# Performance work log

Measured on AMD Instinct MI355X. Metric: run time of the kernel, lower is better.

Reference implementation:

```python
import jax, jax.numpy as jnp
import numpy as np

N = 100000      # nodes
E = 1600000     # edges
IN = 128        # in_channels
HID = 32        # hidden_channels
HEADS = 4
G = 256         # number of graphs in the batch
NEG_SLOPE = 0.2


def setup_inputs() -> dict:
    key = jax.random.key(0)
    ks = jax.random.split(key, 20)
    s = 0.1
    d = {
        'x': jax.random.normal(ks[0], (N, IN), jnp.float32),
        'edge_index': jax.random.randint(ks[1], (2, E), 0, N, dtype=jnp.int64),
        'batch': jnp.sort(jax.random.randint(ks[2], (N,), 0, G, dtype=jnp.int64)),
        # conv1: IN -> HID per head, HEADS heads, concat
        'W1': jax.random.normal(ks[3], (IN, HEADS * HID), jnp.float32) * s,
        'a_src1': jax.random.normal(ks[4], (HEADS, HID), jnp.float32) * s,
        'a_dst1': jax.random.normal(ks[5], (HEADS, HID), jnp.float32) * s,
        'b1': jnp.zeros((HEADS * HID,), jnp.float32),
        # conv2: HEADS*HID -> HID per head, HEADS heads, concat
        'W2': jax.random.normal(ks[6], (HEADS * HID, HEADS * HID), jnp.float32) * s,
        'a_src2': jax.random.normal(ks[7], (HEADS, HID), jnp.float32) * s,
        'a_dst2': jax.random.normal(ks[8], (HEADS, HID), jnp.float32) * s,
        'b2': jnp.zeros((HEADS * HID,), jnp.float32),
        # conv3: HEADS*HID -> HID, 1 head, no concat (mean over heads is identity)
        'W3': jax.random.normal(ks[9], (HEADS * HID, HID), jnp.float32) * s,
        'a_src3': jax.random.normal(ks[10], (1, HID), jnp.float32) * s,
        'a_dst3': jax.random.normal(ks[11], (1, HID), jnp.float32) * s,
        'b3': jnp.zeros((HID,), jnp.float32),
        # final readout
        'fc_w': jax.random.normal(ks[12], (HID, 1), jnp.float32) * s,
        'fc_b': jnp.zeros((1,), jnp.float32),
    }
    return d


def _gat_layer(x, src, dst, W, a_s, a_d, b, concat):
    """One PyG-style GATConv: edge attention logits, per-destination softmax, scatter-aggregate."""
    n = x.shape[0]
    H, C = a_s.shape
    h = (x @ W).reshape(n, H, C)                       # [N, H, C]
    asrc = (h * a_s).sum(-1)                           # [N, H]
    adst = (h * a_d).sum(-1)                           # [N, H]
    e = jax.nn.leaky_relu(asrc[src] + adst[dst], NEG_SLOPE)   # [Etot, H]
    m = jax.ops.segment_max(e, dst, num_segments=n)    # per-dst max (self-loops guarantee non-empty)
    ex = jnp.exp(e - m[dst])
    den = jax.ops.segment_sum(ex, dst, num_segments=n)
    alpha = ex / (den[dst] + 1e-16)                    # segment softmax, [Etot, H]
    out = jax.ops.segment_sum(alpha[:, :, None] * h[src], dst, num_segments=n)  # [N, H, C]
    if concat:
        return out.reshape(n, H * C) + b
    return out.mean(axis=1) + b


def reference(x, edge_index, batch, W1, a_src1, a_dst1, b1, W2, a_src2, a_dst2, b2,
              W3, a_src3, a_dst3, b3, fc_w, fc_b):
    n = x.shape[0]
    loops = jnp.arange(n, dtype=edge_index.dtype)      # GATConv adds self-loops by default
    src = jnp.concatenate([edge_index[0], loops])
    dst = jnp.concatenate([edge_index[1], loops])

    h = jax.nn.elu(_gat_layer(x, src, dst, W1, a_src1, a_dst1, b1, True))
    h = jax.nn.elu(_gat_layer(h, src, dst, W2, a_src2, a_dst2, b2, True))
    h = jax.nn.elu(_gat_layer(h, src, dst, W3, a_src3, a_dst3, b3, False))

    counts = jax.ops.segment_sum(jnp.ones((n,), h.dtype), batch, num_segments=G)
    pooled = jax.ops.segment_sum(h, batch, num_segments=G) / jnp.maximum(counts, 1.0)[:, None]
    # dropout p=0.5 is identity in eval mode
    return pooled @ fc_w + fc_b                        # [G, 1]
```

## Files before the change

kernel.cpp:

```cpp
#include <hip/hip_runtime.h>
#include <hip/hip_bf16.h>
#include <math.h>

#define NEG_SLOPE 0.2f
#define CHUNK 6144

typedef short bf16x8 __attribute__((ext_vector_type(8)));
typedef float f32x4  __attribute__((ext_vector_type(4)));

__device__ __forceinline__ float leaky(float x){ return x > 0.f ? x : NEG_SLOPE*x; }
__device__ __forceinline__ float elu(float x){ return x > 0.f ? x : expm1f(x); }

__device__ __forceinline__ ushort f2bf(float f){
  uint u = __float_as_uint(f);
  u += 0x7fffu + ((u >> 16) & 1u);
  return (ushort)(u >> 16);
}
__device__ __forceinline__ uint pk2(float lo, float hi){
  return (uint)f2bf(lo) | ((uint)f2bf(hi) << 16);
}
__device__ __forceinline__ float2 bfpair(uint v){
  return make_float2(__uint_as_float(v << 16), __uint_as_float(v & 0xffff0000u));
}

__global__ __launch_bounds__(256) void k_histA(const int* __restrict__ ei, int E,
                                               int* __restrict__ bucketCount){
  __shared__ int hist[512];
  for (int b = threadIdx.x; b < 512; b += 256) hist[b] = 0;
  __syncthreads();
  int base = blockIdx.x * 2048;
  int cnt = min(2048, E - base);
  for (int i = threadIdx.x; i < cnt; i += 256)
    atomicAdd(&hist[ei[E + base + i] >> 8], 1);
  __syncthreads();
  for (int b = threadIdx.x; b < 512; b += 256)
    if (hist[b]) atomicAdd(&bucketCount[b], hist[b]);
}

__global__ __launch_bounds__(256) void k_scanB(const int* __restrict__ bucketCount, int NB,
                        int* __restrict__ bucketBase, int* __restrict__ gcursor, int E){
  __shared__ int s[512];
  for (int b = threadIdx.x; b < 512; b += 256)
    s[b] = (b < NB) ? bucketCount[b] : 0;
  __syncthreads();
  if (threadIdx.x == 0){
    int run = 0;
    for (int b = 0; b < NB; b++){ int v = s[b]; s[b] = run; run += v; }
  }
  __syncthreads();
  for (int b = threadIdx.x; b < NB; b += 256){
    bucketBase[b] = s[b]; gcursor[b] = s[b];
  }
  if (threadIdx.x == 0) bucketBase[NB] = E;
}

__global__ __launch_bounds__(256) void k_scatA(const int* __restrict__ ei, int E, int NB,
                         int* __restrict__ gcursor, uint* __restrict__ tmp){
  __shared__ uint stageS[CHUNK];
  __shared__ uint stageD[CHUNK];
  __shared__ int hist[512], pre[512], cur[512], gbase[512];
  __shared__ int scanArr[256];
  int tid = threadIdx.x;
  int base = blockIdx.x * CHUNK;
  int cnt = min(CHUNK, E - base);
  for (int b = tid; b < 512; b += 256) hist[b] = 0;
  __syncthreads();
  for (int i = tid; i < cnt; i += 256)
    atomicAdd(&hist[ei[E + base + i] >> 8], 1);
  __syncthreads();
  int a0 = hist[2*tid], a1 = hist[2*tid+1];
  scanArr[tid] = a0 + a1;
  __syncthreads();
  for (int st = 1; st < 256; st <<= 1){
    int v = (tid >= st) ? scanArr[tid - st] : 0;
    __syncthreads();
    scanArr[tid] += v;
    __syncthreads();
  }
  int eb = tid ? scanArr[tid-1] : 0;
  pre[2*tid] = eb;        cur[2*tid] = eb;
  pre[2*tid+1] = eb + a0; cur[2*tid+1] = eb + a0;
  if (2*tid < NB && a0 > 0)   gbase[2*tid]   = atomicAdd(&gcursor[2*tid],   a0);
  if (2*tid+1 < NB && a1 > 0) gbase[2*tid+1] = atomicAdd(&gcursor[2*tid+1], a1);
  __syncthreads();
  for (int i = tid; i < cnt; i += 256){
    int s = ei[base + i];
    int d = ei[E + base + i];
    int lpos = atomicAdd(&cur[d >> 8], 1);
    stageS[lpos] = (uint)s; stageD[lpos] = (uint)d;
  }
  __syncthreads();
  for (int i = tid; i < cnt; i += 256){
    uint d = stageD[i];
    int b = d >> 8;
    tmp[gbase[b] + (i - pre[b])] = (stageS[i] << 8) | (d & 255u);
  }
}

__global__ __launch_bounds__(256) void k_csr(const uint* __restrict__ tmp,
                      const int* __restrict__ bucketBase,
                      int N, int NB, int* __restrict__ offsets, int* __restrict__ csr){
  int b = blockIdx.x;
  int nodeBase = b << 8;
  int nNodes = min(256, N - nodeBase);
  int eBeg = bucketBase[b], eEnd = bucketBase[b+1];
  __shared__ int deg[256], cur[256];
  int tid = threadIdx.x;
  deg[tid] = 0;
  __syncthreads();
  for (int e = eBeg + tid; e < eEnd; e += 256)
    atomicAdd(&deg[tmp[e] & 255u], 1);
  __syncthreads();
  cur[tid] = deg[tid];
  __syncthreads();
  for (int st = 1; st < 256; st <<= 1){
    int w = (tid >= st) ? cur[tid - st] : 0;
    __syncthreads();
    cur[tid] += w;
    __syncthreads();
  }
  int excl = tid ? cur[tid-1] : 0;
  __syncthreads();
  cur[tid] = excl;
  if (tid < nNodes) offsets[nodeBase + tid] = eBeg + excl;
  if (b == NB-1 && tid == 0) offsets[N] = eEnd;
  __syncthreads();
  for (int e = eBeg + tid; e < eEnd; e += 256){
    uint u = tmp[e];
    int lpos = atomicAdd(&cur[u & 255u], 1);
    csr[eBeg + lpos] = (int)(u >> 8);
  }
}

template<int NT, int H>
__global__ __launch_bounds__(256) void k_wrepA(const float* __restrict__ W,
                    const float* __restrict__ a_s, const float* __restrict__ a_d,
                    ushort* __restrict__ Wf){
  constexpr int NTT = NT + 1;
  constexpr int M = NT*16;
  int idx = blockIdx.x*256 + threadIdx.x;
  if (idx >= NTT*4*64) return;
  int lane = idx & 63;
  int c = (idx >> 6) & 3;
  int t = idx >> 8;
  int j = lane & 15;
  int k0 = c*32 + (lane >> 4)*8;
  float vals[8];
  if (t < NT){
    int col = t*16 + j;
    const float* p0 = W + (size_t)k0*M + col;
    #pragma unroll
    for (int r = 0; r < 8; r++) vals[r] = p0[(size_t)r*M];
  } else {
    #pragma unroll
    for (int r = 0; r < 8; r++) vals[r] = 0.f;
    if (j < 2*H){
      int h = (j < H) ? j : (j - H);
      const float* av = (j < H) ? (a_s + h*32) : (a_d + h*32);
      #pragma unroll
      for (int r = 0; r < 8; r++){
        const float* wr = W + (size_t)(k0 + r)*M + h*32;
        float s = 0.f;
        for (int cc = 0; cc < 32; cc++) s += wr[cc]*av[cc];
        vals[r] = s;
      }
    }
  }
  uint4 o;
  o.x = pk2(vals[0], vals[1]); o.y = pk2(vals[2], vals[3]);
  o.z = pk2(vals[4], vals[5]); o.w = pk2(vals[6], vals[7]);
  *(uint4*)(Wf + (size_t)idx*8) = o;
}

template<int NT, bool A_F32, int H>
__global__ __launch_bounds__(256) void k_mgemm(const void* __restrict__ Xv,
                     const ushort* __restrict__ Wf, ushort* __restrict__ Y,
                     float* __restrict__ asrc, float* __restrict__ adst, int n){
  constexpr int NTT = NT + 1;
  constexpr int M = NT*16;
  int lane = threadIdx.x & 63;
  int l15 = lane & 15, q = lane >> 4;
  int wgid = blockIdx.x*4 + (threadIdx.x >> 6);
  int nchunks = (n + 15) >> 4;
  int stride = gridDim.x*4;

  bf16x8 bw[NTT][4];
  #pragma unroll
  for (int t = 0; t < NTT; t++)
    #pragma unroll
    for (int c = 0; c < 4; c++)
      bw[t][c] = *(const bf16x8*)(Wf + (size_t)(((t<<2)+c)*64 + lane)*8);

  int chunk = wgid;
  if (chunk >= nchunks) return;

  bf16x8 aCur[4], aNext[4];
  auto loadA = [&](int ck, bf16x8* a){
    int m = ck*16 + l15;
    if (m >= n) m = n - 1;
    if (A_F32){
      const float* X = (const float*)Xv + (size_t)m*128 + q*8;
      #pragma unroll
      for (int c = 0; c < 4; c++){
        float4 u0 = *(const float4*)(X + c*32);
        float4 u1 = *(const float4*)(X + c*32 + 4);
        uint4 pkd;
        pkd.x = pk2(u0.x, u0.y); pkd.y = pk2(u0.z, u0.w);
        pkd.z = pk2(u1.x, u1.y); pkd.w = pk2(u1.z, u1.w);
        union { uint4 u; bf16x8 v; } cv; cv.u = pkd;
        a[c] = cv.v;
      }
    } else {
      const ushort* X = (const ushort*)Xv + (size_t)m*128 + q*8;
      #pragma unroll
      for (int c = 0; c < 4; c++) a[c] = *(const bf16x8*)(X + c*32);
    }
  };

  loadA(chunk, aCur);
  while (true){
    int nx = chunk + stride;
    if (nx < nchunks) loadA(nx, aNext);
    f32x4 acc[NTT];
    #pragma unroll
    for (int t = 0; t < NTT; t++) acc[t] = (f32x4){0.f,0.f,0.f,0.f};
    #pragma unroll
    for (int c = 0; c < 4; c++)
      #pragma unroll
      for (int t = 0; t < NTT; t++)
        acc[t] = __builtin_amdgcn_mfma_f32_16x16x32_bf16(aCur[c], bw[t][c], acc[t], 0, 0, 0);
    int rowb = chunk*16 + q*4;
    #pragma unroll
    for (int t = 0; t < NT; t++)
      #pragma unroll
      for (int r = 0; r < 4; r++){
        int row = rowb + r;
        if (row < n) Y[(size_t)row*M + t*16 + l15] = f2bf(acc[t][r]);
      }
    #pragma unroll
    for (int r = 0; r < 4; r++){
      int row = rowb + r;
      if (row < n){
        float v = acc[NT][r];
        if (l15 < H)           asrc[(size_t)row*H + l15]       = v;
        else if (l15 < 2*H)    adst[(size_t)row*H + (l15 - H)] = v;
      }
    }
    if (nx >= nchunks) break;
    chunk = nx;
    #pragma unroll
    for (int c = 0; c < 4; c++) aCur[c] = aNext[c];
  }
}

template<bool OUT_BF16>
__global__ __launch_bounds__(256) void k_agg128f(const ushort* __restrict__ Hb,
                    const float* __restrict__ asrc, const float* __restrict__ adst,
                    const int* __restrict__ offsets, const int* __restrict__ csr_src,
                    const float* __restrict__ bias, void* __restrict__ Out, int n){
  __shared__ float lwAll[4][256];
  int wv = threadIdx.x >> 6;
  int lane = threadIdx.x & 63;
  float* lw = lwAll[wv];
  int node = blockIdx.x*4 + wv;
  if (node >= n) return;
  const int up = lane, ch = up*2, h0 = up >> 4;
  const uint* rows = (const uint*)Hb;
  int j0 = offsets[node], end = offsets[node+1];
  float4 adv = *(const float4*)(adst + (size_t)node*4);
  float adh = (h0==0)?adv.x:(h0==1)?adv.y:(h0==2)?adv.z:adv.w;
  float acc0 = 0.f, acc1 = 0.f, den = 0.f;
  {
    float w = __expf(leaky(asrc[(size_t)node*4 + h0] + adh));
    float2 f = bfpair(rows[(size_t)node*64 + up]);
    den += w; acc0 += w*f.x; acc1 += w*f.y;
  }
  for (int base = j0; base < end; base += 64){
    int m = min(64, end - base);
    int mR = (m + 7) & ~7;
    int sreg = node;
    if (lane < m){
      sreg = csr_src[base + lane];
      float4 a = *(const float4*)(asrc + (size_t)sreg*4);
      float4 w4;
      w4.x = __expf(leaky(a.x + adv.x));
      w4.y = __expf(leaky(a.y + adv.y));
      w4.z = __expf(leaky(a.z + adv.z));
      w4.w = __expf(leaky(a.w + adv.w));
      *(float4*)(lw + lane*4) = w4;
    } else if (lane < mR){
      *(float4*)(lw + lane*4) = make_float4(0.f, 0.f, 0.f, 0.f);
    }
    uint rA[8]; float wA[8];
    uint rB[8]; float wB[8];
    auto loadGroup = [&](int e, uint* r, float* w){
      #pragma unroll
      for (int k = 0; k < 8; k++){
        int s = __builtin_amdgcn_readlane(sreg, e + k);
        r[k] = rows[(size_t)(uint)s*64 + up];
      }
      #pragma unroll
      for (int k = 0; k < 8; k++) w[k] = lw[(e + k)*4 + h0];
    };
    auto consume = [&](const uint* r, const float* w){
      #pragma unroll
      for (int k = 0; k < 8; k++){
        float2 f = bfpair(r[k]);
        den += w[k]; acc0 += w[k]*f.x; acc1 += w[k]*f.y;
      }
    };
    loadGroup(0, rA, wA);
    int e = 8;
    for (; e + 16 <= mR; e += 16){
      loadGroup(e, rB, wB);
      consume(rA, wA);
      loadGroup(e + 8, rA, wA);
      consume(rB, wB);
    }
    if (e < mR){
      loadGroup(e, rB, wB);
      consume(rA, wA);
      consume(rB, wB);
    } else {
      consume(rA, wA);
    }
  }
  float inv = 1.f/(den + 1e-16f);
  float ox = elu(acc0*inv + bias[ch]);
  float oy = elu(acc1*inv + bias[ch+1]);
  if (OUT_BF16){
    ((uint*)Out)[(size_t)node*64 + up] = pk2(ox, oy);
  } else {
    *(float2*)((float*)Out + (size_t)node*128 + ch) = make_float2(ox, oy);
  }
}

__global__ __launch_bounds__(256) void k_agg32(const ushort* __restrict__ Hb,
                    const float* __restrict__ asrc, const float* __restrict__ adst,
                    const int* __restrict__ offsets, const int* __restrict__ csr_src,
                    const float* __restrict__ bias, float* __restrict__ Out, int n){
  __shared__ int   lsAll[4][4][16];
  __shared__ float lwAll[4][4][16];
  int wv = threadIdx.x >> 6;
  int lane = threadIdx.x & 63;
  int g = lane >> 4, i = lane & 15;
  int node = (blockIdx.x*4 + wv)*4 + g;
  if (node >= n) return;
  int* ls = lsAll[wv][g];
  float* lw = lwAll[wv][g];
  const uint* rows = (const uint*)Hb;
  float adn = adst[node];
  float acc0 = 0.f, acc1 = 0.f, den = 0.f;
  {
    float w = __expf(leaky(asrc[node] + adn));
    float2 f = bfpair(rows[(size_t)node*16 + i]);
    den += w; acc0 += w*f.x; acc1 += w*f.y;
  }
  int j0 = offsets[node], end = offsets[node+1];
  for (int base = j0; base < end; base += 16){
    int m = min(16, end - base);
    {
      int idx = base + i;
      bool v = idx < end;
      int s = v ? csr_src[idx] : node;
      ls[i] = s;
      lw[i] = v ? __expf(leaky(asrc[s] + adn)) : 0.f;
    }
    int mR = (m + 3) & ~3;
    for (int e = 0; e < mR; e += 4){
      int s0 = ls[e], s1 = ls[e+1], s2 = ls[e+2], s3 = ls[e+3];
      float w0 = lw[e], w1 = lw[e+1], w2 = lw[e+2], w3 = lw[e+3];
      uint r0 = rows[(size_t)s0*16 + i];
      uint r1 = rows[(size_t)s1*16 + i];
      uint r2 = rows[(size_t)s2*16 + i];
      uint r3 = rows[(size_t)s3*16 + i];
      float2 f0 = bfpair(r0), f1 = bfpair(r1), f2 = bfpair(r2), f3 = bfpair(r3);
      den  += (w0 + w1) + (w2 + w3);
      acc0 += w0*f0.x + w1*f1.x + w2*f2.x + w3*f3.x;
      acc1 += w0*f0.y + w1*f1.y + w2*f2.y + w3*f3.y;
    }
  }
  float inv = 1.f/(den + 1e-16f);
  int ch = i*2;
  float2 o;
  o.x = elu(acc0*inv + bias[ch]);
  o.y = elu(acc1*inv + bias[ch+1]);
  *(float2*)(Out + (size_t)node*32 + ch) = o;
}

__global__ __launch_bounds__(256) void k_bounds(const int* __restrict__ batch, int n, int G,
                                                int* __restrict__ gstart){
  int i = blockIdx.x*256 + threadIdx.x;
  if (i >= n) return;
  int b = batch[i];
  int bp = (i > 0) ? batch[i-1] : -1;
  for (int g = bp + 1; g <= b; g++) gstart[g] = i;
  if (i == n-1){
    for (int g = b + 1; g <= G; g++) gstart[g] = n;
  }
}

__global__ __launch_bounds__(256) void k_pool2(const float* __restrict__ H3,
                     const int* __restrict__ gstart, const float* __restrict__ fcw,
                     const float* __restrict__ fcb, float* __restrict__ out, int G){
  int g = blockIdx.x;
  int s0 = gstart[g], s1 = gstart[g+1];
  int tid = threadIdx.x;
  int c = tid & 31, r = tid >> 5;
  float sum = 0.f;
  for (int i = s0 + r; i < s1; i += 8)
    sum += H3[(size_t)i*32 + c];
  __shared__ float sh[8][32];
  sh[r][c] = sum;
  __syncthreads();
  if (tid < 32){
    float t = 0.f;
    #pragma unroll
    for (int k = 0; k < 8; k++) t += sh[k][tid];
    t *= fcw[tid];
    #pragma unroll
    for (int off = 16; off; off >>= 1) t += __shfl_down(t, off, 32);
    if (tid == 0){
      float cnt = (float)(s1 - s0); if (cnt < 1.f) cnt = 1.f;
      out[g] = t/cnt + fcb[0];
    }
  }
}

extern "C" void kernel_launch(void* const* d_in, const int* in_sizes, int n_in,
                              void* d_out, int out_size, void* d_ws, size_t ws_size,
                              hipStream_t stream){
  const float* x    = (const float*)d_in[0];
  const int*   ei   = (const int*)d_in[1];
  const int*   batch= (const int*)d_in[2];
  const float* W1   = (const float*)d_in[3];
  const float* as1  = (const float*)d_in[4];
  const float* ad1  = (const float*)d_in[5];
  const float* b1   = (const float*)d_in[6];
  const float* W2   = (const float*)d_in[7];
  const float* as2  = (const float*)d_in[8];
  const float* ad2  = (const float*)d_in[9];
  const float* b2   = (const float*)d_in[10];
  const float* W3   = (const float*)d_in[11];
  const float* as3  = (const float*)d_in[12];
  const float* ad3  = (const float*)d_in[13];
  const float* b3   = (const float*)d_in[14];
  const float* fcw  = (const float*)d_in[15];
  const float* fcb  = (const float*)d_in[16];
  float* out = (float*)d_out;

  const int N = in_sizes[0] / 128;
  const int E = in_sizes[1] / 2;
  const int G = out_size;
  const int NB = (N + 255) >> 8;

  char* p = (char*)d_ws;
  auto alloc = [&](size_t bytes) -> void* {
    void* r = (void*)p;
    p += (bytes + 255) & ~(size_t)255;
    return r;
  };
  ushort* bufH   = (ushort*)alloc((size_t)N*128*sizeof(ushort));
  ushort* aggB   = (ushort*)alloc((size_t)N*128*sizeof(ushort));
  float*  bufA32 = (float*)alloc((size_t)N*32*sizeof(float));
  float*  asrc   = (float*)alloc((size_t)N*4*sizeof(float));
  float*  adst   = (float*)alloc((size_t)N*4*sizeof(float));
  int*    offsets= (int*)alloc((size_t)(N+1)*sizeof(int));
  int*    csr    = (int*)alloc((size_t)E*sizeof(int));
  uint*   tmp    = (uint*)alloc((size_t)E*sizeof(uint));
  int*    bCount = (int*)alloc(512*sizeof(int));
  int*    bBase  = (int*)alloc(520*sizeof(int));
  int*    gcursor= (int*)alloc(512*sizeof(int));
  int*    gstart = (int*)alloc((size_t)(G+1)*sizeof(int));
  ushort* Wf1    = (ushort*)alloc(9*4*64*8*sizeof(ushort));
  ushort* Wf2    = (ushort*)alloc(9*4*64*8*sizeof(ushort));
  ushort* Wf3    = (ushort*)alloc(3*4*64*8*sizeof(ushort));

  hipMemsetAsync(bCount, 0, 512*sizeof(int), stream);

  k_wrepA<8,4><<<9, 256, 0, stream>>>(W1, as1, ad1, Wf1);
  k_wrepA<8,4><<<9, 256, 0, stream>>>(W2, as2, ad2, Wf2);
  k_wrepA<2,1><<<3, 256, 0, stream>>>(W3, as3, ad3, Wf3);

  k_histA<<<(E+2047)/2048, 256, 0, stream>>>(ei, E, bCount);
  k_scanB<<<1, 256, 0, stream>>>(bCount, NB, bBase, gcursor, E);
  k_scatA<<<(E+CHUNK-1)/CHUNK, 256, 0, stream>>>(ei, E, NB, gcursor, tmp);
  k_csr<<<NB, 256, 0, stream>>>(tmp, bBase, N, NB, offsets, csr);
  k_bounds<<<(N+255)/256, 256, 0, stream>>>(batch, N, G, gstart);

  const int GB = 512;
  const int NWB = (N + 3)/4;
  const int NWB32 = (N + 15)/16;
  k_mgemm<8, true , 4><<<GB, 256, 0, stream>>>(x, Wf1, bufH, asrc, adst, N);
  k_agg128f<true><<<NWB, 256, 0, stream>>>(bufH, asrc, adst, offsets, csr, b1, aggB, N);
  k_mgemm<8, false, 4><<<GB, 256, 0, stream>>>(aggB, Wf2, bufH, asrc, adst, N);
  k_agg128f<true><<<NWB, 256, 0, stream>>>(bufH, asrc, adst, offsets, csr, b2, aggB, N);
  k_mgemm<2, false, 1><<<GB, 256, 0, stream>>>(aggB, Wf3, bufH, asrc, adst, N);
  k_agg32<<<NWB32, 256, 0, stream>>>(bufH, asrc, adst, offsets, csr, b3, bufA32, N);
  k_pool2<<<G, 256, 0, stream>>>(bufA32, gstart, fcw, fcb, out, G);
}
```

Baseline: 448.5 us.

## Fuse layer-3 aggregation with pooling readout, merge weight-prep kernels, resize GEMM grid

Layer-3 aggregation now applies the fc weights in place and reduces each node's 32 channels to one scalar. That scalar is atomically added into a per-graph pool buffer split 16 ways, so the N×32 float intermediate and the separate pooling pass are no longer needed. A small finalize kernel divides by the node count and adds the bias. The three weight-preparation launches are merged into one, the GEMM grid is sized so each wave handles exactly one 16-row chunk, and separate asrc/adst buffers are used per layer. Atomic float accumulation makes the output order-dependent and may cause contention on graphs with many nodes.

```diff
diff --git a/kernel.cpp b/kernel.cpp
--- a/kernel.cpp
+++ b/kernel.cpp
@@ -133,12 +133,11 @@
 }
 
 template<int NT, int H>
-__global__ __launch_bounds__(256) void k_wrepA(const float* __restrict__ W,
+__device__ __forceinline__ void wrep_dev(const float* __restrict__ W,
                     const float* __restrict__ a_s, const float* __restrict__ a_d,
-                    ushort* __restrict__ Wf){
+                    ushort* __restrict__ Wf, int idx){
   constexpr int NTT = NT + 1;
   constexpr int M = NT*16;
-  int idx = blockIdx.x*256 + threadIdx.x;
   if (idx >= NTT*4*64) return;
   int lane = idx & 63;
   int c = (idx >> 6) & 3;
@@ -170,6 +169,16 @@
   o.x = pk2(vals[0], vals[1]); o.y = pk2(vals[2], vals[3]);
   o.z = pk2(vals[4], vals[5]); o.w = pk2(vals[6], vals[7]);
   *(uint4*)(Wf + (size_t)idx*8) = o;
+}
+
+__global__ __launch_bounds__(256) void k_wrepAll(
+    const float* __restrict__ W1, const float* __restrict__ as1, const float* __restrict__ ad1, ushort* __restrict__ Wf1,
+    const float* __restrict__ W2, const float* __restrict__ as2, const float* __restrict__ ad2, ushort* __restrict__ Wf2,
+    const float* __restrict__ W3, const float* __restrict__ as3, const float* __restrict__ ad3, ushort* __restrict__ Wf3){
+  int b = blockIdx.x;
+  if (b < 9)       wrep_dev<8,4>(W1, as1, ad1, Wf1, b*256 + threadIdx.x);
+  else if (b < 18) wrep_dev<8,4>(W2, as2, ad2, Wf2, (b-9)*256 + threadIdx.x);
+  else             wrep_dev<2,1>(W3, as3, ad3, Wf3, (b-18)*256 + threadIdx.x);
 }
 
 template<int NT, bool A_F32, int H>
@@ -335,10 +344,11 @@
   }
 }
 
-__global__ __launch_bounds__(256) void k_agg32(const ushort* __restrict__ Hb,
+__global__ __launch_bounds__(256) void k_agg32pool(const ushort* __restrict__ Hb,
                     const float* __restrict__ asrc, const float* __restrict__ adst,
                     const int* __restrict__ offsets, const int* __restrict__ csr_src,
-                    const float* __restrict__ bias, float* __restrict__ Out, int n){
+                    const float* __restrict__ bias, const float* __restrict__ fcw,
+                    const int* __restrict__ batch, float* __restrict__ pool, int n){
   __shared__ int   lsAll[4][4][16];
   __shared__ float lwAll[4][4][16];
   int wv = threadIdx.x >> 6;
@@ -382,10 +392,11 @@
   }
   float inv = 1.f/(den + 1e-16f);
   int ch = i*2;
-  float2 o;
-  o.x = elu(acc0*inv + bias[ch]);
-  o.y = elu(acc1*inv + bias[ch+1]);
-  *(float2*)(Out + (size_t)node*32 + ch) = o;
+  float2 fw = *(const float2*)(fcw + ch);
+  float t = elu(acc0*inv + bias[ch])*fw.x + elu(acc1*inv + bias[ch+1])*fw.y;
+  #pragma unroll
+  for (int off = 1; off < 16; off <<= 1) t += __shfl_xor(t, off, 16);
+  if (i == 0) atomicAdd(&pool[(size_t)batch[node]*16 + (node & 15)], t);
 }
 
 __global__ __launch_bounds__(256) void k_bounds(const int* __restrict__ batch, int n, int G,
@@ -400,31 +411,17 @@
   }
 }
 
-__global__ __launch_bounds__(256) void k_pool2(const float* __restrict__ H3,
-                     const int* __restrict__ gstart, const float* __restrict__ fcw,
-                     const float* __restrict__ fcb, float* __restrict__ out, int G){
-  int g = blockIdx.x;
-  int s0 = gstart[g], s1 = gstart[g+1];
-  int tid = threadIdx.x;
-  int c = tid & 31, r = tid >> 5;
-  float sum = 0.f;
-  for (int i = s0 + r; i < s1; i += 8)
-    sum += H3[(size_t)i*32 + c];
-  __shared__ float sh[8][32];
-  sh[r][c] = sum;
-  __syncthreads();
-  if (tid < 32){
-    float t = 0.f;
-    #pragma unroll
-    for (int k = 0; k < 8; k++) t += sh[k][tid];
-    t *= fcw[tid];
-    #pragma unroll
-    for (int off = 16; off; off >>= 1) t += __shfl_down(t, off, 32);
-    if (tid == 0){
-      float cnt = (float)(s1 - s0); if (cnt < 1.f) cnt = 1.f;
-      out[g] = t/cnt + fcb[0];
-    }
-  }
+__global__ __launch_bounds__(256) void k_poolfin(const float* __restrict__ pool,
+                    const int* __restrict__ gstart, const float* __restrict__ fcb,
+                    float* __restrict__ out, int G){
+  int g = blockIdx.x*256 + threadIdx.x;
+  if (g >= G) return;
+  float s = 0.f;
+  #pragma unroll
+  for (int k = 0; k < 16; k++) s += pool[(size_t)g*16 + k];
+  float cnt = (float)(gstart[g+1] - gstart[g]);
+  if (cnt < 1.f) cnt = 1.f;
+  out[g] = s/cnt + fcb[0];
 }
 
 extern "C" void kernel_launch(void* const* d_in, const int* in_sizes, int n_in,
@@ -462,9 +459,11 @@
   };
   ushort* bufH   = (ushort*)alloc((size_t)N*128*sizeof(ushort));
   ushort* aggB   = (ushort*)alloc((size_t)N*128*sizeof(ushort));
-  float*  bufA32 = (float*)alloc((size_t)N*32*sizeof(float));
-  float*  asrc   = (float*)alloc((size_t)N*4*sizeof(float));
-  float*  adst   = (float*)alloc((size_t)N*4*sizeof(float));
+  ushort* bufH3  = (ushort*)alloc((size_t)N*32*sizeof(ushort));
+  float*  asrcA  = (float*)alloc((size_t)N*4*sizeof(float));
+  float*  adstA  = (float*)alloc((size_t)N*4*sizeof(float));
+  float*  asrcB  = (float*)alloc((size_t)N*4*sizeof(float));
+  float*  adstB  = (float*)alloc((size_t)N*4*sizeof(float));
   int*    offsets= (int*)alloc((size_t)(N+1)*sizeof(int));
   int*    csr    = (int*)alloc((size_t)E*sizeof(int));
   uint*   tmp    = (uint*)alloc((size_t)E*sizeof(uint));
@@ -472,15 +471,15 @@
   int*    bBase  = (int*)alloc(520*sizeof(int));
   int*    gcursor= (int*)alloc(512*sizeof(int));
   int*    gstart = (int*)alloc((size_t)(G+1)*sizeof(int));
+  float*  pool   = (float*)alloc((size_t)G*16*sizeof(float));
   ushort* Wf1    = (ushort*)alloc(9*4*64*8*sizeof(ushort));
   ushort* Wf2    = (ushort*)alloc(9*4*64*8*sizeof(ushort));
   ushort* Wf3    = (ushort*)alloc(3*4*64*8*sizeof(ushort));
 
   hipMemsetAsync(bCount, 0, 512*sizeof(int), stream);
-
-  k_wrepA<8,4><<<9, 256, 0, stream>>>(W1, as1, ad1, Wf1);
-  k_wrepA<8,4><<<9, 256, 0, stream>>>(W2, as2, ad2, Wf2);
-  k_wrepA<2,1><<<3, 256, 0, stream>>>(W3, as3, ad3, Wf3);
+  hipMemsetAsync(pool, 0, (size_t)G*16*sizeof(float), stream);
+
+  k_wrepAll<<<21, 256, 0, stream>>>(W1, as1, ad1, Wf1, W2, as2, ad2, Wf2, W3, as3, ad3, Wf3);
 
   k_histA<<<(E+2047)/2048, 256, 0, stream>>>(ei, E, bCount);
   k_scanB<<<1, 256, 0, stream>>>(bCount, NB, bBase, gcursor, E);
@@ -488,14 +487,15 @@
   k_csr<<<NB, 256, 0, stream>>>(tmp, bBase, N, NB, offsets, csr);
   k_bounds<<<(N+255)/256, 256, 0, stream>>>(batch, N, G, gstart);
 
-  const int GB = 512;
+  const int GB = (((N + 15)/16) + 3)/4;
   const int NWB = (N + 3)/4;
   const int NWB32 = (N + 15)/16;
-  k_mgemm<8, true , 4><<<GB, 256, 0, stream>>>(x, Wf1, bufH, asrc, adst, N);
-  k_agg128f<true><<<NWB, 256, 0, stream>>>(bufH, asrc, adst, offsets, csr, b1, aggB, N);
-  k_mgemm<8, false, 4><<<GB, 256, 0, stream>>>(aggB, Wf2, bufH, asrc, adst, N);
-  k_agg128f<true><<<NWB, 256, 0, stream>>>(bufH, asrc, adst, offsets, csr, b2, aggB, N);
-  k_mgemm<2, false, 1><<<GB, 256, 0, stream>>>(aggB, Wf3, bufH, asrc, adst, N);
-  k_agg32<<<NWB32, 256, 0, stream>>>(bufH, asrc, adst, offsets, csr, b3, bufA32, N);
-  k_pool2<<<G, 256, 0, stream>>>(bufA32, gstart, fcw, fcb, out, G);
-}
+  k_mgemm<8, true , 4><<<GB, 256, 0, stream>>>(x, Wf1, bufH, asrcA, adstA, N);
+  k_agg128f<true><<<NWB, 256, 0, stream>>>(bufH, asrcA, adstA, offsets, csr, b1, aggB, N);
+  k_mgemm<8, false, 4><<<GB, 256, 0, stream>>>(aggB, Wf2, bufH, asrcB, adstB, N);
+  k_agg128f<true><<<NWB, 256, 0, stream>>>(bufH, asrcB, adstB, offsets, csr, b2, aggB, N);
+  k_mgemm<2, false, 1><<<GB, 256, 0, stream>>>(aggB, Wf3, bufH3, asrcA, adstA, N);
+  k_agg32pool<<<NWB32, 256, 0, stream>>>(bufH3, asrcA, adstA, offsets, csr,
+                                         b3, fcw, batch, pool, N);
+  k_poolfin<<<(G+255)/256, 256, 0, stream>>>(pool, gstart, fcb, out, G);
+}
```

After: 433.6 us. 3.3% less time.
